# Performance work log

Hardware: AMD Instinct MI355X
Metric: run time of the kernel (lower is better)

The kernel has to match this reference:

```python
import jax, jax.numpy as jnp
import numpy as np

NUM_HEADS = 12

def _rotate_half(t):
    t1, t2 = jnp.split(t, 2, axis=-1)
    return jnp.concatenate([-t2, t1], axis=-1)

def _rope_apply(t, sin, cos):
    # t: [B,H,N,Dh]; sin/cos: [N,Dh] broadcast over B,H
    return t * cos + _rotate_half(t) * sin


def setup_inputs() -> dict:
    key = jax.random.key(0)
    ks = jax.random.split(key, 6)
    B, N, D = 2, 2048, 768
    Dh = D // NUM_HEADS
    return {
        "x": jax.random.normal(ks[0], (B, N, D), dtype=jnp.float32),
        "sin": jax.random.uniform(ks[1], (N, Dh), dtype=jnp.float32),
        "cos": jax.random.uniform(ks[2], (N, Dh), dtype=jnp.float32),
        "qkv_w": jax.random.normal(ks[3], (3 * D, D), dtype=jnp.float32) * (D ** -0.5),
        "proj_w": jax.random.normal(ks[4], (D, D), dtype=jnp.float32) * (D ** -0.5),
        "proj_b": jax.random.normal(ks[5], (D,), dtype=jnp.float32),
    }


def reference(x, sin, cos, qkv_w, proj_w, proj_b):
    B, N, D = x.shape
    H = NUM_HEADS
    Dh = D // H
    scale = Dh ** -0.5
    # fused QKV projection (qkv_bias=False)
    qkv = jnp.einsum("bnd,ed->bne", x, qkv_w)              # [B,N,3D]
    qkv = qkv.reshape(B, N, 3, H, Dh)
    q = jnp.transpose(qkv[:, :, 0], (0, 2, 1, 3))          # [B,H,N,Dh]
    k = jnp.transpose(qkv[:, :, 1], (0, 2, 1, 3))
    v = jnp.transpose(qkv[:, :, 2], (0, 2, 1, 3))
    # inline RoPE (prefix = 0: sin/cos cover all N positions)
    q = _rope_apply(q, sin, cos)
    k = _rope_apply(k, sin, cos)
    # scaled dot-product attention
    scores = jnp.einsum("bhqd,bhkd->bhqk", q, k) * scale   # [B,H,N,N]
    attn = jax.nn.softmax(scores, axis=-1)
    out = jnp.einsum("bhqk,bhkd->bhqd", attn, v)           # [B,H,N,Dh]
    out = jnp.transpose(out, (0, 2, 1, 3)).reshape(B, N, D)
    # output projection
    return jnp.einsum("bnd,ed->bne", out, proj_w) + proj_b
```

## Files before the change

kernel.cpp:

```cpp
#include <hip/hip_runtime.h>
#include <hip/hip_bf16.h>
#include <stdint.h>


typedef unsigned short u16;
typedef __attribute__((ext_vector_type(8))) short s16x8;
typedef __attribute__((ext_vector_type(4))) short s16x4;
typedef __attribute__((ext_vector_type(4))) float f32x4;

#define MFMA16(a, b, c) __builtin_amdgcn_mfma_f32_16x16x32_bf16((a), (b), (c), 0, 0, 0)

__device__ __forceinline__ f32x4 mfma_k16(s16x4 a, s16x4 b, f32x4 c) {
    asm("s_nop 3\n\tv_mfma_f32_16x16x16_bf16 %0, %1, %2, %0"
        : "+v"(c) : "v"(a), "v"(b));
    return c;
}

__device__ __forceinline__ u16 f2bf(float f) {
    uint32_t u = __float_as_uint(f);
    u = u + 0x7fffu + ((u >> 16) & 1u);
    return (u16)(u >> 16);
}
__device__ __forceinline__ uint32_t pk2(float lo, float hi) {
    return (uint32_t)f2bf(lo) | ((uint32_t)f2bf(hi) << 16);
}
__device__ __forceinline__ uint32_t pk2t(float lo, float hi) {
    return __builtin_amdgcn_perm(__float_as_uint(hi), __float_as_uint(lo),
                                 0x07060302u);
}
__device__ __forceinline__ float fexp2(float x) { return __builtin_amdgcn_exp2f(x); }

__device__ __forceinline__ void gload16(const void* g, void* l) {
    __builtin_amdgcn_global_load_lds(
        (const __attribute__((address_space(1))) unsigned int*)g,
        (__attribute__((address_space(3))) unsigned int*)l,
        16, 0, 0);
}

__global__ __launch_bounds__(256)
void k_cvt3(const float* __restrict__ s0, const float* __restrict__ s1,
            const float* __restrict__ s2, u16* __restrict__ dst,
            int a, int ab, int tot)
{
    const int i = blockIdx.x * 256 + threadIdx.x;
    if (i >= tot) return;
    const float4* src;
    if (i < a)       src = (const float4*)s0 + i;
    else if (i < ab) src = (const float4*)s1 + (i - a);
    else             src = (const float4*)s2 + (i - ab);
    const float4 v = *src;
    ushort4 o;
    o.x = f2bf(v.x); o.y = f2bf(v.y); o.z = f2bf(v.z); o.w = f2bf(v.w);
    ((ushort4*)dst)[i] = o;
}

__global__ __launch_bounds__(256, 2)
void k_qkv_rope(const u16* __restrict__ X,
                const u16* __restrict__ W,
                const float* __restrict__ SIN,
                const float* __restrict__ COS,
                u16* __restrict__ qws, u16* __restrict__ kws, u16* __restrict__ vtws)
{
    __shared__ u16 smem[17408];
    u16* const As0 = smem;
    u16* const Bs0 = smem + 8192;

    const int t  = threadIdx.x;
    const int l  = t & 63;
    const int w  = t >> 6;
    const int cl = l & 15, gh = l >> 4;
    const int brow = blockIdx.x * 128;
    const int bcol = blockIdx.y * 128;
    const int wr = (w >> 1) * 64;
    const int wc = (w & 1) * 64;

    const int srow = w * 16 + (l >> 2);
    const int scol = (((l & 3) ^ ((l >> 3) & 3)) * 8);
    const u16* gA = X + (size_t)(brow + srow) * 768 + scol;
    const u16* gB = W + (size_t)(bcol + srow) * 768 + scol;

    const int csw = ((cl >> 1) & 3);

    f32x4 acc[4][4] = {};

    gload16(gA,            As0 + w * 512);
    gload16(gA + 64 * 768, As0 + 2048 + w * 512);
    gload16(gB,            Bs0 + w * 512);
    gload16(gB + 64 * 768, Bs0 + 2048 + w * 512);
    __syncthreads();

    for (int kt = 0; kt < 24; ++kt) {
        const int cur = kt & 1;
        if (kt + 1 < 24) {
            const int k0 = (kt + 1) * 32;
            u16* An = As0 + (cur ^ 1) * 4096;
            u16* Bn = Bs0 + (cur ^ 1) * 4096;
            gload16(gA + k0,            An + w * 512);
            gload16(gA + k0 + 64 * 768, An + 2048 + w * 512);
            gload16(gB + k0,            Bn + w * 512);
            gload16(gB + k0 + 64 * 768, Bn + 2048 + w * 512);
        }
        const char* Ac = (const char*)(As0 + cur * 4096);
        const char* Bc = (const char*)(Bs0 + cur * 4096);
        s16x8 af[4], bv[4];
        #pragma unroll
        for (int m = 0; m < 4; ++m) {
            const int row = wr + m * 16 + cl;
            af[m] = *(const s16x8*)(Ac + row * 64 + ((gh ^ csw) << 4));
        }
        #pragma unroll
        for (int n = 0; n < 4; ++n) {
            const int row = wc + n * 16 + cl;
            bv[n] = *(const s16x8*)(Bc + row * 64 + ((gh ^ csw) << 4));
        }
        #pragma unroll
        for (int m = 0; m < 4; ++m)
            #pragma unroll
            for (int n = 0; n < 4; ++n)
                acc[m][n] = MFMA16(af[m], bv[n], acc[m][n]);
        __syncthreads();
    }

    if (blockIdx.y >= 12) {
        u16* const Vt = smem;
        #pragma unroll
        for (int m = 0; m < 4; ++m)
            #pragma unroll
            for (int jj = 0; jj < 4; ++jj) {
                const int rowl = wr + m * 16 + gh * 4 + jj;
                #pragma unroll
                for (int n = 0; n < 4; ++n)
                    Vt[(wc + n * 16 + cl) * 136 + rowl] = f2bf(acc[m][n][jj]);
            }
        __syncthreads();
        const int dhcol = t >> 1;
        const int c     = t & 1;
        const int gcol  = bcol + dhcol;
        const int h     = (gcol >> 6) - 24;
        const int dh    = gcol & 63;
        const int b     = brow >> 11;
        const int tok0  = (brow & 2047) + c * 64;
        u16* dst = vtws + ((size_t)(b * 12 + h) * 64 + dh) * 2048 + tok0;
        const uint4* src = (const uint4*)((const char*)Vt + dhcol * 272 + c * 128);
        #pragma unroll
        for (int j = 0; j < 8; ++j)
            ((uint4*)dst)[j] = src[j];
    } else {
        const int seg   = (bcol + wc) >> 6;
        const int which = seg / 12;
        const int h     = seg % 12;
        const float qscl = (which == 0) ? 0.1803368801111244f : 1.0f;
        u16* outp = (which == 0) ? qws : kws;

        #pragma unroll
        for (int m = 0; m < 4; ++m) {
            #pragma unroll
            for (int jj = 0; jj < 4; ++jj) {
                const int row = brow + wr + m * 16 + gh * 4 + jj;
                const int b   = row >> 11;
                const int tok = row & 2047;
                u16* orow = outp + ((size_t)(b * 12 + h) * 2048 + tok) * 64;
                const float* srow2 = SIN + tok * 64;
                const float* crow2 = COS + tok * 64;
                #pragma unroll
                for (int n = 0; n < 4; ++n) {
                    const int dh = n * 16 + cl;
                    const float v = acc[m][n][jj];
                    const float partner = (n < 2) ? -acc[m][n + 2][jj] : acc[m][n - 2][jj];
                    orow[dh] = f2bf((v * crow2[dh] + partner * srow2[dh]) * qscl);
                }
            }
        }
    }
}

__global__ __launch_bounds__(256)
void k_attn(const u16* __restrict__ Qg, const u16* __restrict__ Kg,
            const u16* __restrict__ VTg, u16* __restrict__ Og)
{
    __shared__ u16 Ks[2][64 * 64];
    __shared__ u16 Vs[2][64 * 64];

    const int t  = threadIdx.x;
    const int l  = t & 63;
    const int w  = t >> 6;
    const int cl = l & 15, gh = l >> 4;

    const int i  = blockIdx.x;
    const int bh = (i & 7) * 3 + ((i >> 3) % 3);
    const int qt = i / 24;
    const int qb = qt * 64 + w * 16;

    const u16* Q  = Qg  + (size_t)bh * 2048 * 64;
    const char* Kb  = (const char*)(Kg  + (size_t)bh * 2048 * 64);
    const char* VTb = (const char*)(VTg + (size_t)bh * 64 * 2048);

    s16x8 qf[2];
    #pragma unroll
    for (int ks = 0; ks < 2; ++ks)
        qf[ks] = *(const s16x8*)(Q + (((qb + cl) << 6) + ks * 32 + gh * 8));

    f32x4 o[4] = {};
    float lrun = 0.f;

    const int srow8 = l >> 3;
    const int scolb = (((l & 7) ^ srow8) << 4);
    const int rsw = (cl & 7) << 4;

    {
        #pragma unroll
        for (int c = 0; c < 2; ++c) {
            const int s = c * 4 + w;
            const int grow = s * 8 + srow8;
            gload16(Kb  + grow * 128 + scolb,  &Ks[0][s * 512]);
            gload16(VTb + grow * 4096 + scolb, &Vs[0][s * 512]);
        }
    }
    __syncthreads();

    for (int kt = 0; kt < 32; ++kt) {
        const int cur = kt & 1;

        if (kt + 1 < 32) {
            const int nb = (kt + 1) * 64;
            #pragma unroll
            for (int c = 0; c < 2; ++c) {
                const int s = c * 4 + w;
                const int grow = s * 8 + srow8;
                gload16(Kb  + (nb + grow) * 128 + scolb,    &Ks[cur ^ 1][s * 512]);
                gload16(VTb + grow * 4096 + nb * 2 + scolb, &Vs[cur ^ 1][s * 512]);
            }
        }

        const char* kl = (const char*)Ks[cur];
        const char* vl = (const char*)Vs[cur];
        s16x8 kf[4][2];
        s16x4 vf[4][4];
        #pragma unroll
        for (int nk = 0; nk < 4; ++nk)
            #pragma unroll
            for (int ks = 0; ks < 2; ++ks)
                kf[nk][ks] = *(const s16x8*)(kl + (nk * 16 + cl) * 128 + ((ks * 64 + gh * 16) ^ rsw));
        #pragma unroll
        for (int n = 0; n < 4; ++n)
            #pragma unroll
            for (int nk = 0; nk < 4; ++nk)
                vf[n][nk] = *(const s16x4*)(vl + (n * 16 + cl) * 128 + ((nk * 32 + gh * 8) ^ rsw));

        f32x4 st[4];
        #pragma unroll
        for (int nk = 0; nk < 4; ++nk)
            #pragma unroll
            for (int jj = 0; jj < 4; ++jj)
                st[nk][jj] = -12.f;
        #pragma unroll
        for (int nk = 0; nk < 4; ++nk)
            #pragma unroll
            for (int ks = 0; ks < 2; ++ks)
                st[nk] = MFMA16(kf[nk][ks], qf[ks], st[nk]);

        union { uint32_t u[2]; s16x4 v; } pd[4];
        float sum = 0.f;
        #pragma unroll
        for (int nk = 0; nk < 4; ++nk) {
            const float p0 = fexp2(st[nk][0]);
            const float p1 = fexp2(st[nk][1]);
            const float p2 = fexp2(st[nk][2]);
            const float p3 = fexp2(st[nk][3]);
            sum += (p0 + p1) + (p2 + p3);
            pd[nk].u[0] = pk2t(p0, p1);
            pd[nk].u[1] = pk2t(p2, p3);
        }
        lrun += sum;

        #pragma unroll
        for (int nk = 0; nk < 4; ++nk)
            #pragma unroll
            for (int n = 0; n < 4; ++n)
                o[n] = mfma_k16(vf[n][nk], pd[nk].v, o[n]);

        __syncthreads();
    }

    const int b = bh / 12, h = bh % 12;
    float lr = lrun;
    lr += __shfl_xor(lr, 16);
    lr += __shfl_xor(lr, 32);
    const float inv = 1.0f / lr;
    const int tok = qb + cl;
    u16* orow = Og + ((size_t)(b * 2048 + tok)) * 768 + h * 64;
    #pragma unroll
    for (int n = 0; n < 4; ++n) {
        uint2 pkv;
        pkv.x = pk2(o[n][0] * inv, o[n][1] * inv);
        pkv.y = pk2(o[n][2] * inv, o[n][3] * inv);
        *(uint2*)(orow + n * 16 + gh * 4) = pkv;
    }
}

__global__ __launch_bounds__(256, 2)
void k_proj(const u16* __restrict__ A,
            const u16* __restrict__ W,
            const float* __restrict__ BIAS,
            float* __restrict__ OUT)
{
    __shared__ u16 smem[16384];
    u16* const As0 = smem;
    u16* const Bs0 = smem + 8192;

    const int t  = threadIdx.x;
    const int l  = t & 63;
    const int w  = t >> 6;
    const int cl = l & 15, gh = l >> 4;
    const int brow = blockIdx.x * 128;
    const int bcol = blockIdx.y * 128;
    const int wr = (w >> 1) * 64;
    const int wc = (w & 1) * 64;

    const int srow = w * 16 + (l >> 2);
    const int scol = (((l & 3) ^ ((l >> 3) & 3)) * 8);
    const u16* gA = A + (size_t)(brow + srow) * 768 + scol;
    const u16* gB = W + (size_t)(bcol + srow) * 768 + scol;
    const int csw = ((cl >> 1) & 3);

    f32x4 acc[4][4] = {};

    gload16(gA,            As0 + w * 512);
    gload16(gA + 64 * 768, As0 + 2048 + w * 512);
    gload16(gB,            Bs0 + w * 512);
    gload16(gB + 64 * 768, Bs0 + 2048 + w * 512);
    __syncthreads();

    for (int kt = 0; kt < 24; ++kt) {
        const int cur = kt & 1;
        if (kt + 1 < 24) {
            const int k0 = (kt + 1) * 32;
            u16* An = As0 + (cur ^ 1) * 4096;
            u16* Bn = Bs0 + (cur ^ 1) * 4096;
            gload16(gA + k0,            An + w * 512);
            gload16(gA + k0 + 64 * 768, An + 2048 + w * 512);
            gload16(gB + k0,            Bn + w * 512);
            gload16(gB + k0 + 64 * 768, Bn + 2048 + w * 512);
        }
        const char* Ac = (const char*)(As0 + cur * 4096);
        const char* Bc = (const char*)(Bs0 + cur * 4096);
        s16x8 af[4], bv[4];
        #pragma unroll
        for (int m = 0; m < 4; ++m) {
            const int row = wr + m * 16 + cl;
            af[m] = *(const s16x8*)(Ac + row * 64 + ((gh ^ csw) << 4));
        }
        #pragma unroll
        for (int n = 0; n < 4; ++n) {
            const int row = wc + n * 16 + cl;
            bv[n] = *(const s16x8*)(Bc + row * 64 + ((gh ^ csw) << 4));
        }
        #pragma unroll
        for (int m = 0; m < 4; ++m)
            #pragma unroll
            for (int n = 0; n < 4; ++n)
                acc[m][n] = MFMA16(af[m], bv[n], acc[m][n]);
        __syncthreads();
    }

    #pragma unroll
    for (int m = 0; m < 4; ++m) {
        #pragma unroll
        for (int jj = 0; jj < 4; ++jj) {
            const int row = brow + wr + m * 16 + gh * 4 + jj;
            #pragma unroll
            for (int n = 0; n < 4; ++n) {
                const int col = bcol + wc + n * 16 + cl;
                OUT[(size_t)row * 768 + col] = acc[m][n][jj] + BIAS[col];
            }
        }
    }
}

extern "C" void kernel_launch(void* const* d_in, const int* in_sizes, int n_in,
                              void* d_out, int out_size, void* d_ws, size_t ws_size,
                              hipStream_t stream)
{
    const float* x     = (const float*)d_in[0];
    const float* sinp  = (const float*)d_in[1];
    const float* cosp  = (const float*)d_in[2];
    const float* qkv_w = (const float*)d_in[3];
    const float* projw = (const float*)d_in[4];
    const float* projb = (const float*)d_in[5];
    float* out = (float*)d_out;

    const size_t N_X  = (size_t)4096 * 768;
    const size_t N_WQ = (size_t)2304 * 768;
    const size_t N_WP = (size_t)768 * 768;
    const size_t SEG  = (size_t)2 * 12 * 2048 * 64;

    u16* xbf   = (u16*)d_ws;
    u16* wqkv  = xbf + N_X;
    u16* wproj = wqkv + N_WQ;
    u16* qws   = wproj + N_WP;
    u16* kws   = qws + SEG;
    u16* vtws  = kws + SEG;
    u16* aws   = vtws + SEG;

    const int a   = (int)(N_X / 4);
    const int ab  = (int)((N_X + N_WQ) / 4);
    const int tot = (int)((N_X + N_WQ + N_WP) / 4);
    k_cvt3<<<(tot + 255) / 256, 256, 0, stream>>>(x, qkv_w, projw, xbf, a, ab, tot);

    k_qkv_rope<<<dim3(32, 18), 256, 0, stream>>>(xbf, wqkv, sinp, cosp, qws, kws, vtws);
    k_attn    <<<768, 256, 0, stream>>>(qws, kws, vtws, aws);
    k_proj    <<<dim3(32, 6),  256, 0, stream>>>(aws, wproj, projb, out);
}
```

Measured before the change: 94.27 us.

## Split attention KV tile across waves, each wave covering all query rows

```diff
diff --git a/kernel.cpp b/kernel.cpp
--- a/kernel.cpp
+++ b/kernel.cpp
@@ -174,7 +174,7 @@
     }
 }
 
-__global__ __launch_bounds__(256)
+__global__ __launch_bounds__(256, 3)
 void k_attn(const u16* __restrict__ Qg, const u16* __restrict__ Kg,
             const u16* __restrict__ VTg, u16* __restrict__ Og)
 {
@@ -189,19 +189,21 @@
     const int i  = blockIdx.x;
     const int bh = (i & 7) * 3 + ((i >> 3) % 3);
     const int qt = i / 24;
-    const int qb = qt * 64 + w * 16;
+    const int qb = qt * 64;
 
     const u16* Q  = Qg  + (size_t)bh * 2048 * 64;
     const char* Kb  = (const char*)(Kg  + (size_t)bh * 2048 * 64);
     const char* VTb = (const char*)(VTg + (size_t)bh * 64 * 2048);
 
-    s16x8 qf[2];
+    s16x8 qf[4][2];
     #pragma unroll
-    for (int ks = 0; ks < 2; ++ks)
-        qf[ks] = *(const s16x8*)(Q + (((qb + cl) << 6) + ks * 32 + gh * 8));
-
-    f32x4 o[4] = {};
-    float lrun = 0.f;
+    for (int m = 0; m < 4; ++m)
+        #pragma unroll
+        for (int ks = 0; ks < 2; ++ks)
+            qf[m][ks] = *(const s16x8*)(Q + (((qb + m * 16 + cl) << 6) + ks * 32 + gh * 8));
+
+    f32x4 o[4][4] = {};
+    float lrun[4] = {};
 
     const int srow8 = l >> 3;
     const int scolb = (((l & 7) ^ srow8) << 4);
@@ -234,67 +236,80 @@
 
         const char* kl = (const char*)Ks[cur];
         const char* vl = (const char*)Vs[cur];
-        s16x8 kf[4][2];
-        s16x4 vf[4][4];
-        #pragma unroll
-        for (int nk = 0; nk < 4; ++nk)
+        s16x8 kf[2];
+        s16x4 vf[4];
+        #pragma unroll
+        for (int ks = 0; ks < 2; ++ks)
+            kf[ks] = *(const s16x8*)(kl + (w * 16 + cl) * 128 + ((ks * 64 + gh * 16) ^ rsw));
+        #pragma unroll
+        for (int n = 0; n < 4; ++n)
+            vf[n] = *(const s16x4*)(vl + (n * 16 + cl) * 128 + ((w * 32 + gh * 8) ^ rsw));
+
+        f32x4 st[4];
+        #pragma unroll
+        for (int m = 0; m < 4; ++m)
+            #pragma unroll
+            for (int jj = 0; jj < 4; ++jj)
+                st[m][jj] = -12.f;
+        #pragma unroll
+        for (int m = 0; m < 4; ++m)
             #pragma unroll
             for (int ks = 0; ks < 2; ++ks)
-                kf[nk][ks] = *(const s16x8*)(kl + (nk * 16 + cl) * 128 + ((ks * 64 + gh * 16) ^ rsw));
+                st[m] = MFMA16(kf[ks], qf[m][ks], st[m]);
+
+        union { uint32_t u[2]; s16x4 v; } pd[4];
+        #pragma unroll
+        for (int m = 0; m < 4; ++m) {
+            const float p0 = fexp2(st[m][0]);
+            const float p1 = fexp2(st[m][1]);
+            const float p2 = fexp2(st[m][2]);
+            const float p3 = fexp2(st[m][3]);
+            lrun[m] += (p0 + p1) + (p2 + p3);
+            pd[m].u[0] = pk2t(p0, p1);
+            pd[m].u[1] = pk2t(p2, p3);
+        }
+
         #pragma unroll
         for (int n = 0; n < 4; ++n)
             #pragma unroll
-            for (int nk = 0; nk < 4; ++nk)
-                vf[n][nk] = *(const s16x4*)(vl + (n * 16 + cl) * 128 + ((nk * 32 + gh * 8) ^ rsw));
-
-        f32x4 st[4];
-        #pragma unroll
-        for (int nk = 0; nk < 4; ++nk)
-            #pragma unroll
-            for (int jj = 0; jj < 4; ++jj)
-                st[nk][jj] = -12.f;
-        #pragma unroll
-        for (int nk = 0; nk < 4; ++nk)
-            #pragma unroll
-            for (int ks = 0; ks < 2; ++ks)
-                st[nk] = MFMA16(kf[nk][ks], qf[ks], st[nk]);
-
-        union { uint32_t u[2]; s16x4 v; } pd[4];
-        float sum = 0.f;
-        #pragma unroll
-        for (int nk = 0; nk < 4; ++nk) {
-            const float p0 = fexp2(st[nk][0]);
-            const float p1 = fexp2(st[nk][1]);
-            const float p2 = fexp2(st[nk][2]);
-            const float p3 = fexp2(st[nk][3]);
-            sum += (p0 + p1) + (p2 + p3);
-            pd[nk].u[0] = pk2t(p0, p1);
-            pd[nk].u[1] = pk2t(p2, p3);
-        }
-        lrun += sum;
-
-        #pragma unroll
-        for (int nk = 0; nk < 4; ++nk)
-            #pragma unroll
-            for (int n = 0; n < 4; ++n)
-                o[n] = mfma_k16(vf[n][nk], pd[nk].v, o[n]);
-
-        __syncthreads();
-    }
-
+            for (int m = 0; m < 4; ++m)
+                o[n][m] = mfma_k16(vf[n], pd[m].v, o[n][m]);
+
+        __syncthreads();
+    }
+
+    f32x4* OL = (f32x4*)&Ks[0][0];
+    float*  ML = (float*)&Vs[0][0];
     const int b = bh / 12, h = bh % 12;
-    float lr = lrun;
-    lr += __shfl_xor(lr, 16);
-    lr += __shfl_xor(lr, 32);
-    const float inv = 1.0f / lr;
-    const int tok = qb + cl;
-    u16* orow = Og + ((size_t)(b * 2048 + tok)) * 768 + h * 64;
+
     #pragma unroll
-    for (int n = 0; n < 4; ++n) {
+    for (int m = 0; m < 4; ++m) {
+        float lr = lrun[m];
+        lr += __shfl_xor(lr, 16);
+        lr += __shfl_xor(lr, 32);
+        ML[(m * 4 + w) * 64 + l] = lr;
+    }
+
+    #pragma unroll
+    for (int m = 0; m < 4; ++m) {
+        __syncthreads();
+        #pragma unroll
+        for (int n = 0; n < 4; ++n)
+            OL[(n * 4 + w) * 64 + l] = o[n][m];
+        __syncthreads();
+        f32x4 oacc = OL[(w * 4 + 0) * 64 + l];
+        oacc += OL[(w * 4 + 1) * 64 + l];
+        oacc += OL[(w * 4 + 2) * 64 + l];
+        oacc += OL[(w * 4 + 3) * 64 + l];
+        const float lt = ML[(m * 4 + 0) * 64 + l] + ML[(m * 4 + 1) * 64 + l]
+                       + ML[(m * 4 + 2) * 64 + l] + ML[(m * 4 + 3) * 64 + l];
+        const float inv = 1.0f / lt;
+        const int tok = qb + m * 16 + cl;
+        u16* orow = Og + ((size_t)(b * 2048 + tok)) * 768 + h * 64 + w * 16 + gh * 4;
         uint2 pkv;
-        pkv.x = pk2(o[n][0] * inv, o[n][1] * inv);
-        pkv.y = pk2(o[n][2] * inv, o[n][3] * inv);
-        *(uint2*)(orow + n * 16 + gh * 4) = pkv;
+        pkv.x = pk2(oacc[0] * inv, oacc[1] * inv);
+        pkv.y = pk2(oacc[2] * inv, oacc[3] * inv);
+        *(uint2*)orow = pkv;
     }
 }
 
```

After: 93.97 us. Within noise of the previous version (-0.3%).
